# Optimization experiments

Measured on AMD Instinct MI355X. Metric: run time of the kernel, lower is better.

## Reference

```python
import jax, jax.numpy as jnp
import numpy as np

BATCH = 4096
IN_SIZES = [1024, 1024, 1024, 1024]
EMB = 2048  # embracement_size


def setup_inputs() -> dict:
    key = jax.random.key(0)
    keys = jax.random.split(key, 3 * len(IN_SIZES))
    inp = {}
    for i, d in enumerate(IN_SIZES):
        inp[f"x{i}"] = jax.random.normal(keys[3 * i], (BATCH, d), dtype=jnp.float32)
        # Linear params (Kaiming-ish scale)
        inp[f"W{i}"] = jax.random.normal(keys[3 * i + 1], (d, EMB), dtype=jnp.float32) / np.sqrt(d)
        inp[f"b{i}"] = jax.random.normal(keys[3 * i + 2], (EMB,), dtype=jnp.float32) * 0.01
    return inp


def _sample_indices(batch, num_feats, emb):
    # availabilities=None, selection_probabilities=None -> uniform p over modalities
    # multinomial(p, num_samples=emb, replacement=True) == categorical over log p
    logits = jnp.zeros((batch, num_feats), dtype=jnp.float32)  # uniform
    k = jax.random.key(42)
    # shape (emb, batch) broadcasts against logits batch shape (batch,)
    idx = jax.random.categorical(k, logits, axis=-1, shape=(emb, batch))
    return idx.T  # [batch, emb]


def reference(x0, W0, b0, x1, W1, b1, x2, W2, b2, x3, W3, b3):
    xs = [x0, x1, x2, x3]
    Ws = [W0, W1, W2, W3]
    bs = [b0, b1, b2, b3]
    # docking: Linear + ReLU per modality -> [batch, EMB, num_feats]
    dock = jnp.stack([jax.nn.relu(x @ W + b) for x, W, b in zip(xs, Ws, bs)], axis=-1)
    B, E, F = dock.shape
    idx = _sample_indices(B, F, E)  # [B, E] int32
    # gather along modality axis (replaces one-hot multiply-sum)
    out = jnp.take_along_axis(dock, idx[:, :, None], axis=-1)[..., 0]
    return out  # [batch, EMB]
```

## Files before the change

kernel.cpp:

```cpp
#include <hip/hip_runtime.h>
#include <stdint.h>


typedef short short8 __attribute__((ext_vector_type(8)));
typedef float floatx4 __attribute__((ext_vector_type(4)));

#define B_DIM 4096
#define K_DIM 1024
#define E_DIM 2048

__device__ __forceinline__ uint16_t f2bf(float x) {
  uint32_t u = __float_as_uint(x);
  u += 0x7FFFu + ((u >> 16) & 1u);
  return (uint16_t)(u >> 16);
}

__device__ __forceinline__ void threefry(uint32_t x0, uint32_t x1,
                                         uint32_t& o0, uint32_t& o1) {
  const uint32_t ks0 = 0u;
  const uint32_t ks1 = 42u;
  const uint32_t ks2 = 0x1BD11BDAu ^ 42u;
  x0 += ks0; x1 += ks1;
#define TF_R(r) { x0 += x1; x1 = (x1 << r) | (x1 >> (32 - r)); x1 ^= x0; }
  TF_R(13) TF_R(15) TF_R(26) TF_R(6)
  x0 += ks1; x1 += ks2 + 1u;
  TF_R(17) TF_R(29) TF_R(16) TF_R(24)
  x0 += ks2; x1 += ks0 + 2u;
  TF_R(13) TF_R(15) TF_R(26) TF_R(6)
  x0 += ks0; x1 += ks1 + 3u;
  TF_R(17) TF_R(29) TF_R(16) TF_R(24)
  x0 += ks1; x1 += ks2 + 4u;
  TF_R(13) TF_R(15) TF_R(26) TF_R(6)
  x0 += ks2; x1 += ks0 + 5u;
#undef TF_R
  o0 = x0; o1 = x1;
}

__global__ __launch_bounds__(256) void idx_kernel(uint32_t* __restrict__ idx2) {
  uint32_t tid = blockIdx.x * 256u + threadIdx.x;
  uint32_t base = tid << 6;
  uint32_t word = 0;
#pragma unroll 2
  for (int j = 0; j < 16; ++j) {
    uint32_t c = base + 4u * j;
    uint32_t best = 0, bi = 0;
#pragma unroll
    for (uint32_t f = 0; f < 4; ++f) {
      uint32_t y0, y1;
      threefry(0u, c + f, y0, y1);
      uint32_t m = (y0 ^ y1) >> 9;
      if (f == 0) best = m;
      else if (m > best) { best = m; bi = f; }
    }
    word |= bi << (2 * j);
  }
  idx2[tid] = word;
}

__global__ __launch_bounds__(256) void convert_x(
    const float* __restrict__ x0, const float* __restrict__ x1,
    const float* __restrict__ x2, const float* __restrict__ x3,
    uint16_t* __restrict__ xb) {
  int f = blockIdx.z;
  const float* x = (f == 0) ? x0 : (f == 1) ? x1 : (f == 2) ? x2 : x3;
  size_t i = ((size_t)blockIdx.x * 256 + threadIdx.x) * 4;
  float4 v = *(const float4*)(x + i);
  union { uint16_t h[4]; uint64_t q; } p;
  p.h[0] = f2bf(v.x); p.h[1] = f2bf(v.y);
  p.h[2] = f2bf(v.z); p.h[3] = f2bf(v.w);
  *(uint64_t*)(xb + (size_t)f * B_DIM * K_DIM + i) = p.q;
}

__global__ __launch_bounds__(256) void convert_w(
    const float* __restrict__ W0, const float* __restrict__ W1,
    const float* __restrict__ W2, const float* __restrict__ W3,
    uint16_t* __restrict__ Wt) {
  __shared__ float tile[32][33];
  int f = blockIdx.z;
  const float* W = (f == 0) ? W0 : (f == 1) ? W1 : (f == 2) ? W2 : W3;
  int e0 = blockIdx.x * 32, k0 = blockIdx.y * 32;
  int tx = threadIdx.x, ty = threadIdx.y;
#pragma unroll
  for (int i = 0; i < 4; ++i)
    tile[ty + i * 8][tx] = W[(size_t)(k0 + ty + i * 8) * E_DIM + e0 + tx];
  __syncthreads();
  uint16_t* dst = Wt + (size_t)f * E_DIM * K_DIM;
#pragma unroll
  for (int i = 0; i < 4; ++i)
    dst[(size_t)(e0 + ty + i * 8) * K_DIM + k0 + tx] = f2bf(tile[tx][ty + i * 8]);
}

__device__ __forceinline__ void async16(const uint16_t* g, uint16_t* lds) {
  __builtin_amdgcn_global_load_lds(
      (const __attribute__((address_space(1))) void*)g,
      (__attribute__((address_space(3))) void*)lds, 16, 0, 0);
}

__global__ __launch_bounds__(256, 2) void gemm_fused(
    const uint16_t* __restrict__ Ab, const uint16_t* __restrict__ Bbt,
    const uint32_t* __restrict__ idx2,
    const float* __restrict__ bias0, const float* __restrict__ bias1,
    const float* __restrict__ bias2, const float* __restrict__ bias3,
    float* __restrict__ out) {
  __shared__ uint16_t As[128 * 32];
  __shared__ uint16_t Bs[128 * 32];

  const int tid = threadIdx.x;
  const int w = tid >> 6;
  const int l = tid & 63;
  const int mBase = blockIdx.y * 128;
  const int nBase = blockIdx.x * 128;

  const int wm = (w >> 1) * 64, wn = (w & 1) * 64;
  const int ar = l >> 2, ac8 = l & 3;
  const int fr = l & 15, fq = l >> 4;

  const int b_hi0 = (mBase + wm) >> 4;
  uint32_t iw[4][4];
#pragma unroll
  for (int ni = 0; ni < 4; ++ni) {
    int col = nBase + wn + ni * 16 + fr;
#pragma unroll
    for (int mi = 0; mi < 4; ++mi)
      iw[ni][mi] = idx2[(size_t)col * (B_DIM / 16) + b_hi0 + mi];
  }

  floatx4 res[4][4] = {};

#pragma unroll 1
  for (int f = 0; f < 4; ++f) {
    const uint16_t* A = Ab  + (size_t)f * B_DIM * K_DIM + (size_t)mBase * K_DIM;
    const uint16_t* B = Bbt + (size_t)f * E_DIM * K_DIM + (size_t)nBase * K_DIM;

    floatx4 acc[4][4] = {};
    for (int k0 = 0; k0 < K_DIM; k0 += 32) {
      #pragma unroll
      for (int t = 0; t < 2; ++t) {
        int c = w * 2 + t;
        async16(A + (size_t)(c * 16 + ar) * K_DIM + k0 + ac8 * 8, &As[c * 512]);
        async16(B + (size_t)(c * 16 + ar) * K_DIM + k0 + ac8 * 8, &Bs[c * 512]);
      }
      __syncthreads();

      short8 a[4], b[4];
      #pragma unroll
      for (int mi = 0; mi < 4; ++mi)
        a[mi] = *(const short8*)&As[(wm + mi * 16 + fr) * 32 + fq * 8];
      #pragma unroll
      for (int ni = 0; ni < 4; ++ni)
        b[ni] = *(const short8*)&Bs[(wn + ni * 16 + fr) * 32 + fq * 8];
      #pragma unroll
      for (int mi = 0; mi < 4; ++mi)
        #pragma unroll
        for (int ni = 0; ni < 4; ++ni)
          acc[mi][ni] = __builtin_amdgcn_mfma_f32_16x16x32_bf16(
              a[mi], b[ni], acc[mi][ni], 0, 0, 0);
      __syncthreads();
    }

    const float* bias = (f == 0) ? bias0 : (f == 1) ? bias1
                      : (f == 2) ? bias2 : bias3;
    #pragma unroll
    for (int ni = 0; ni < 4; ++ni) {
      float bvf = bias[nBase + wn + ni * 16 + fr];
      #pragma unroll
      for (int mi = 0; mi < 4; ++mi) {
        uint32_t wd = iw[ni][mi];
        #pragma unroll
        for (int r = 0; r < 4; ++r) {
          uint32_t sel = (wd >> (2 * (fq * 4 + r))) & 3u;
          if (sel == (uint32_t)f) res[mi][ni][r] = acc[mi][ni][r] + bvf;
        }
      }
    }
  }

#pragma unroll
  for (int ni = 0; ni < 4; ++ni) {
    int col = nBase + wn + ni * 16 + fr;
#pragma unroll
    for (int mi = 0; mi < 4; ++mi) {
      int row0 = mBase + wm + mi * 16 + fq * 4;
#pragma unroll
      for (int r = 0; r < 4; ++r) {
        float o = res[mi][ni][r];
        __builtin_nontemporal_store(o > 0.f ? o : 0.f,
                                    &out[(size_t)(row0 + r) * E_DIM + col]);
      }
    }
  }
}

extern "C" void kernel_launch(void* const* d_in, const int* in_sizes, int n_in,
                              void* d_out, int out_size, void* d_ws, size_t ws_size,
                              hipStream_t stream) {
  const float* x[4]; const float* W[4]; const float* bs[4];
  for (int f = 0; f < 4; ++f) {
    x[f]  = (const float*)d_in[3 * f + 0];
    W[f]  = (const float*)d_in[3 * f + 1];
    bs[f] = (const float*)d_in[3 * f + 2];
  }
  char* ws = (char*)d_ws;
  uint16_t* xb  = (uint16_t*)ws;
  uint16_t* Wt  = (uint16_t*)(ws + (size_t)32 * 1024 * 1024);
  uint32_t* idx2 = (uint32_t*)(ws + (size_t)48 * 1024 * 1024);
  float* out = (float*)d_out;

  idx_kernel<<<dim3(2048), dim3(256), 0, stream>>>(idx2);
  convert_x<<<dim3(4096, 1, 4), dim3(256), 0, stream>>>(x[0], x[1], x[2], x[3], xb);
  convert_w<<<dim3(64, 32, 4), dim3(32, 8), 0, stream>>>(W[0], W[1], W[2], W[3], Wt);
  gemm_fused<<<dim3(E_DIM / 128, B_DIM / 128), dim3(256), 0, stream>>>(
      xb, Wt, idx2, bs[0], bs[1], bs[2], bs[3], out);
}
```

Baseline: 309.2 us.

## Double-buffer GEMM LDS with 512-thread blocks and merge conversion kernels

The GEMM now uses 8 waves per 128x128 tile, each owning a 64x32 sub-tile. A/B tiles are double-buffered in LDS so the next K-slice's async load is issued before the current slice's MFMAs, which removes one barrier per iteration. The x and W conversion kernels are merged into a single launch, and the W transpose now writes 8-byte vectorized stores. The idx kernel unroll is also raised; the trade-off is more LDS per block and fewer MFMAs per wave between LDS reads.

```diff
diff --git a/kernel.cpp b/kernel.cpp
--- a/kernel.cpp
+++ b/kernel.cpp
@@ -40,7 +40,7 @@
   uint32_t tid = blockIdx.x * 256u + threadIdx.x;
   uint32_t base = tid << 6;
   uint32_t word = 0;
-#pragma unroll 2
+#pragma unroll 4
   for (int j = 0; j < 16; ++j) {
     uint32_t c = base + 4u * j;
     uint32_t best = 0, bi = 0;
@@ -57,37 +57,40 @@
   idx2[tid] = word;
 }
 
-__global__ __launch_bounds__(256) void convert_x(
+__global__ __launch_bounds__(256) void convert_all(
     const float* __restrict__ x0, const float* __restrict__ x1,
     const float* __restrict__ x2, const float* __restrict__ x3,
-    uint16_t* __restrict__ xb) {
-  int f = blockIdx.z;
-  const float* x = (f == 0) ? x0 : (f == 1) ? x1 : (f == 2) ? x2 : x3;
-  size_t i = ((size_t)blockIdx.x * 256 + threadIdx.x) * 4;
-  float4 v = *(const float4*)(x + i);
-  union { uint16_t h[4]; uint64_t q; } p;
-  p.h[0] = f2bf(v.x); p.h[1] = f2bf(v.y);
-  p.h[2] = f2bf(v.z); p.h[3] = f2bf(v.w);
-  *(uint64_t*)(xb + (size_t)f * B_DIM * K_DIM + i) = p.q;
-}
-
-__global__ __launch_bounds__(256) void convert_w(
     const float* __restrict__ W0, const float* __restrict__ W1,
     const float* __restrict__ W2, const float* __restrict__ W3,
-    uint16_t* __restrict__ Wt) {
-  __shared__ float tile[32][33];
-  int f = blockIdx.z;
-  const float* W = (f == 0) ? W0 : (f == 1) ? W1 : (f == 2) ? W2 : W3;
-  int e0 = blockIdx.x * 32, k0 = blockIdx.y * 32;
-  int tx = threadIdx.x, ty = threadIdx.y;
-#pragma unroll
-  for (int i = 0; i < 4; ++i)
-    tile[ty + i * 8][tx] = W[(size_t)(k0 + ty + i * 8) * E_DIM + e0 + tx];
-  __syncthreads();
-  uint16_t* dst = Wt + (size_t)f * E_DIM * K_DIM;
-#pragma unroll
-  for (int i = 0; i < 4; ++i)
-    dst[(size_t)(e0 + ty + i * 8) * K_DIM + k0 + tx] = f2bf(tile[tx][ty + i * 8]);
+    uint16_t* __restrict__ xb, uint16_t* __restrict__ Wt) {
+  int z = blockIdx.z;
+  if (z < 4) {
+    const float* x = (z == 0) ? x0 : (z == 1) ? x1 : (z == 2) ? x2 : x3;
+    size_t i = ((size_t)blockIdx.x * 256 + threadIdx.x) * 4;
+    float4 v = *(const float4*)(x + i);
+    union { uint16_t h[4]; uint64_t q; } p;
+    p.h[0] = f2bf(v.x); p.h[1] = f2bf(v.y);
+    p.h[2] = f2bf(v.z); p.h[3] = f2bf(v.w);
+    *(uint64_t*)(xb + (size_t)z * B_DIM * K_DIM + i) = p.q;
+  } else {
+    if (blockIdx.x >= 2048) return;
+    int f = z - 4;
+    const float* W = (f == 0) ? W0 : (f == 1) ? W1 : (f == 2) ? W2 : W3;
+    __shared__ float tile[32][33];
+    int e0 = (blockIdx.x & 63) * 32, k0 = (blockIdx.x >> 6) * 32;
+    int tx = threadIdx.x & 31, ty = threadIdx.x >> 5;
+#pragma unroll
+    for (int i = 0; i < 4; ++i)
+      tile[ty + i * 8][tx] = W[(size_t)(k0 + ty + i * 8) * E_DIM + e0 + tx];
+    __syncthreads();
+    int t = threadIdx.x;
+    int el = t >> 3, kc = (t & 7) * 4;
+    union { uint16_t h[4]; uint64_t q; } p;
+#pragma unroll
+    for (int i = 0; i < 4; ++i) p.h[i] = f2bf(tile[kc + i][el]);
+    uint16_t* dst = Wt + (size_t)f * E_DIM * K_DIM;
+    *(uint64_t*)(dst + (size_t)(e0 + el) * K_DIM + k0 + kc) = p.q;
+  }
 }
 
 __device__ __forceinline__ void async16(const uint16_t* g, uint16_t* lds) {
@@ -96,14 +99,14 @@
       (__attribute__((address_space(3))) void*)lds, 16, 0, 0);
 }
 
-__global__ __launch_bounds__(256, 2) void gemm_fused(
+__global__ __launch_bounds__(512, 4) void gemm_fused(
     const uint16_t* __restrict__ Ab, const uint16_t* __restrict__ Bbt,
     const uint32_t* __restrict__ idx2,
     const float* __restrict__ bias0, const float* __restrict__ bias1,
     const float* __restrict__ bias2, const float* __restrict__ bias3,
     float* __restrict__ out) {
-  __shared__ uint16_t As[128 * 32];
-  __shared__ uint16_t Bs[128 * 32];
+  __shared__ uint16_t As[2][128 * 32];
+  __shared__ uint16_t Bs[2][128 * 32];
 
   const int tid = threadIdx.x;
   const int w = tid >> 6;
@@ -111,57 +114,65 @@
   const int mBase = blockIdx.y * 128;
   const int nBase = blockIdx.x * 128;
 
-  const int wm = (w >> 1) * 64, wn = (w & 1) * 64;
-  const int ar = l >> 2, ac8 = l & 3;
+  const int wm = (w >> 2) * 64;
+  const int wn = (w & 3) * 32;
+  const int sr = l >> 2, sc8 = l & 3;
   const int fr = l & 15, fq = l >> 4;
 
   const int b_hi0 = (mBase + wm) >> 4;
-  uint32_t iw[4][4];
-#pragma unroll
-  for (int ni = 0; ni < 4; ++ni) {
+  uint32_t iw[2][4];
+#pragma unroll
+  for (int ni = 0; ni < 2; ++ni) {
     int col = nBase + wn + ni * 16 + fr;
 #pragma unroll
     for (int mi = 0; mi < 4; ++mi)
       iw[ni][mi] = idx2[(size_t)col * (B_DIM / 16) + b_hi0 + mi];
   }
 
-  floatx4 res[4][4] = {};
+  floatx4 res[4][2] = {};
 
 #pragma unroll 1
   for (int f = 0; f < 4; ++f) {
     const uint16_t* A = Ab  + (size_t)f * B_DIM * K_DIM + (size_t)mBase * K_DIM;
     const uint16_t* B = Bbt + (size_t)f * E_DIM * K_DIM + (size_t)nBase * K_DIM;
-
-    floatx4 acc[4][4] = {};
-    for (int k0 = 0; k0 < K_DIM; k0 += 32) {
-      #pragma unroll
-      for (int t = 0; t < 2; ++t) {
-        int c = w * 2 + t;
-        async16(A + (size_t)(c * 16 + ar) * K_DIM + k0 + ac8 * 8, &As[c * 512]);
-        async16(B + (size_t)(c * 16 + ar) * K_DIM + k0 + ac8 * 8, &Bs[c * 512]);
+    const uint16_t* Aw = A + (size_t)(16 * w + sr) * K_DIM + sc8 * 8;
+    const uint16_t* Bw = B + (size_t)(16 * w + sr) * K_DIM + sc8 * 8;
+
+    floatx4 acc[4][2] = {};
+
+    async16(Aw, &As[0][w * 512]);
+    async16(Bw, &Bs[0][w * 512]);
+    __syncthreads();
+
+    int buf = 0;
+#pragma unroll 1
+    for (int kt = 0; kt < 32; ++kt) {
+      int k0 = kt * 32;
+      if (kt + 1 < 32) {
+        async16(Aw + k0 + 32, &As[buf ^ 1][w * 512]);
+        async16(Bw + k0 + 32, &Bs[buf ^ 1][w * 512]);
       }
-      __syncthreads();
-
-      short8 a[4], b[4];
+      short8 a[4], b[2];
       #pragma unroll
       for (int mi = 0; mi < 4; ++mi)
-        a[mi] = *(const short8*)&As[(wm + mi * 16 + fr) * 32 + fq * 8];
-      #pragma unroll
-      for (int ni = 0; ni < 4; ++ni)
-        b[ni] = *(const short8*)&Bs[(wn + ni * 16 + fr) * 32 + fq * 8];
+        a[mi] = *(const short8*)&As[buf][(wm + mi * 16 + fr) * 32 + fq * 8];
+      #pragma unroll
+      for (int ni = 0; ni < 2; ++ni)
+        b[ni] = *(const short8*)&Bs[buf][(wn + ni * 16 + fr) * 32 + fq * 8];
       #pragma unroll
       for (int mi = 0; mi < 4; ++mi)
         #pragma unroll
-        for (int ni = 0; ni < 4; ++ni)
+        for (int ni = 0; ni < 2; ++ni)
           acc[mi][ni] = __builtin_amdgcn_mfma_f32_16x16x32_bf16(
               a[mi], b[ni], acc[mi][ni], 0, 0, 0);
       __syncthreads();
+      buf ^= 1;
     }
 
     const float* bias = (f == 0) ? bias0 : (f == 1) ? bias1
                       : (f == 2) ? bias2 : bias3;
     #pragma unroll
-    for (int ni = 0; ni < 4; ++ni) {
+    for (int ni = 0; ni < 2; ++ni) {
       float bvf = bias[nBase + wn + ni * 16 + fr];
       #pragma unroll
       for (int mi = 0; mi < 4; ++mi) {
@@ -176,7 +187,7 @@
   }
 
 #pragma unroll
-  for (int ni = 0; ni < 4; ++ni) {
+  for (int ni = 0; ni < 2; ++ni) {
     int col = nBase + wn + ni * 16 + fr;
 #pragma unroll
     for (int mi = 0; mi < 4; ++mi) {
@@ -207,8 +218,8 @@
   float* out = (float*)d_out;
 
   idx_kernel<<<dim3(2048), dim3(256), 0, stream>>>(idx2);
-  convert_x<<<dim3(4096, 1, 4), dim3(256), 0, stream>>>(x[0], x[1], x[2], x[3], xb);
-  convert_w<<<dim3(64, 32, 4), dim3(32, 8), 0, stream>>>(W[0], W[1], W[2], W[3], Wt);
-  gemm_fused<<<dim3(E_DIM / 128, B_DIM / 128), dim3(256), 0, stream>>>(
+  convert_all<<<dim3(4096, 1, 8), dim3(256), 0, stream>>>(
+      x[0], x[1], x[2], x[3], W[0], W[1], W[2], W[3], xb, Wt);
+  gemm_fused<<<dim3(E_DIM / 128, B_DIM / 128), dim3(512), 0, stream>>>(
       xb, Wt, idx2, bs[0], bs[1], bs[2], bs[3], out);
 }
```

New measurement: 306.2 us. About the same (-1.0%).
